# Kernel tuning notes

Hardware: AMD Instinct MI355X
Metric: run time of the kernel (lower is better)

The kernel has to match this reference:

```python
import jax, jax.numpy as jnp
import numpy as np

B, T, C = 4, 2048, 1024  # n_embd == input_size == 1024
H, D = 16, 64            # num_heads, head_size


def setup_inputs() -> dict:
    key = jax.random.key(0)
    ks = jax.random.split(key, 5)
    s_in = (1.0 / C) ** 0.5   # ~Linear default init scale
    s_pr = (1.0 / (H * D)) ** 0.5
    return {
        "x": jax.random.normal(ks[0], (B, T, C), dtype=jnp.float32),
        "wq": jax.random.normal(ks[1], (H, C, D), dtype=jnp.float32) * s_in,
        "wk": jax.random.normal(ks[2], (H, C, D), dtype=jnp.float32) * s_in,
        "wv": jax.random.normal(ks[3], (H, C, D), dtype=jnp.float32) * s_in,
        "w_proj": jax.random.normal(ks[4], (H * D, C), dtype=jnp.float32) * s_pr,
        "b_proj": jnp.zeros((C,), dtype=jnp.float32),
    }


def reference(x, wq, wk, wv, w_proj, b_proj):
    Bb, Tt, Cc = x.shape
    # Batched per-head projections: [B,T,C] x [H,C,D] -> [B,H,T,D]
    q = jnp.einsum("btc,hcd->bhtd", x, wq)
    k = jnp.einsum("btc,hcd->bhtd", x, wk)
    v = jnp.einsum("btc,hcd->bhtd", x, wv)
    # NOTE: original scales by C**-0.5 with C = full embedding dim (quirk preserved)
    scale = Cc ** (-0.5)
    scores = jnp.einsum("bhtd,bhsd->bhts", q, k) * scale  # [B,H,T,T]
    causal = jnp.tril(jnp.ones((Tt, Tt), dtype=bool))
    scores = jnp.where(causal, scores, -jnp.inf)
    wei = jax.nn.softmax(scores, axis=-1)
    out = jnp.einsum("bhts,bhsd->bhtd", wei, v)           # [B,H,T,D]
    out = out.transpose(0, 2, 1, 3).reshape(Bb, Tt, -1)    # concat heads [B,T,H*D]
    return out @ w_proj + b_proj                           # [B,T,C]
```

## Files before the change

kernel.cpp:

```cpp
#include <hip/hip_runtime.h>
#include <stdint.h>


typedef uint32_t u32;
typedef __bf16 bf16x8 __attribute__((ext_vector_type(8)));
typedef __bf16 bf16x4 __attribute__((ext_vector_type(4)));
typedef unsigned short us8 __attribute__((ext_vector_type(8)));
typedef float f32x4 __attribute__((ext_vector_type(4)));

#define EXP2F(x) __builtin_amdgcn_exp2f(x)

static __device__ __forceinline__ unsigned short f2bf(float f) {
  union { float f; u32 i; } cv; cv.f = f;
  u32 x = cv.i;
  u32 r = (x + 0x7fffu + ((x >> 16) & 1u)) >> 16;
  return (unsigned short)r;
}

static __device__ __forceinline__ void gload_lds16(const unsigned short* g, unsigned short* l) {
  __builtin_amdgcn_global_load_lds(
      (__attribute__((address_space(1))) u32*)g,
      (__attribute__((address_space(3))) u32*)l, 16, 0, 0);
}

#define G8_LGKM do { asm volatile("s_waitcnt lgkmcnt(0)" ::: "memory"); \
                     __builtin_amdgcn_sched_barrier(0); } while (0)

__global__ __launch_bounds__(256) void prep(
    const float* __restrict__ x, const float* __restrict__ wq,
    const float* __restrict__ wk, const float* __restrict__ wv,
    const float* __restrict__ wp, unsigned short* __restrict__ x_bf,
    unsigned short* __restrict__ wtq, unsigned short* __restrict__ wtp) {
  __shared__ unsigned short lds[64][66];
  const int b = blockIdx.x, tid = threadIdx.x;
  if (b < 4096) {
    size_t i = (size_t)(b * 256 + tid) * 8u;
    float4 a = *(const float4*)(x + i);
    float4 c = *(const float4*)(x + i + 4);
    us8 v;
    v[0] = f2bf(a.x); v[1] = f2bf(a.y); v[2] = f2bf(a.z); v[3] = f2bf(a.w);
    v[4] = f2bf(c.x); v[5] = f2bf(c.y); v[6] = f2bf(c.z); v[7] = f2bf(c.w);
    *(us8*)(x_bf + i) = v;
    return;
  }
  if (b < 4864) {
    int idx = b - 4096;
    int z = idx >> 8, rem = idx & 255;
    int h = rem >> 4, c0 = (rem & 15) << 6;
    const float* src = (z == 0) ? wq : (z == 1) ? wk : wv;
    unsigned short* d = wtq + ((size_t)z << 20);
    const float* s = src + (size_t)h * 65536u + (size_t)c0 * 64u;
#pragma unroll
    for (int it = 0; it < 16; ++it) {
      int i2 = it * 256 + tid;
      int r = i2 >> 6, dd = i2 & 63;
      lds[dd][r] = f2bf(s[r * 64 + dd]);
    }
    __syncthreads();
#pragma unroll
    for (int it = 0; it < 16; ++it) {
      int i2 = it * 256 + tid;
      int dd = i2 >> 6, r = i2 & 63;
      d[(size_t)(h * 64 + dd) * 1024u + c0 + r] = lds[dd][r];
    }
    return;
  }
  {
    int idx = b - 4864;
    int c0 = (idx >> 4) << 6, r0 = (idx & 15) << 6;
#pragma unroll
    for (int it = 0; it < 16; ++it) {
      int i2 = it * 256 + tid;
      int r = i2 >> 6, cc = i2 & 63;
      lds[cc][r] = f2bf(wp[(size_t)(r0 + r) * 1024u + c0 + cc]);
    }
    __syncthreads();
#pragma unroll
    for (int it = 0; it < 16; ++it) {
      int i2 = it * 256 + tid;
      int cc = i2 >> 6, r = i2 & 63;
      wtp[(size_t)(c0 + cc) * 1024u + r0 + r] = lds[cc][r];
    }
  }
}

static __device__ __forceinline__ void gn_stage(const unsigned short* g,
                                                unsigned short* d, int tid) {
#pragma unroll
  for (int l = 0; l < 4; ++l) {
    int cid = l * 256 + tid;
    int r = cid >> 3, c = cid & 7;
    gload_lds16(g + (size_t)r * 1024 + ((c ^ (r & 7)) << 3), d + cid * 8);
  }
}
static __device__ __forceinline__ void gn_ldA(bf16x8 af[4][2], const unsigned short* As,
                                              int wr, int l15, int lhi) {
#pragma unroll
  for (int mi = 0; mi < 4; ++mi)
#pragma unroll
    for (int ks = 0; ks < 2; ++ks) {
      int row = wr * 64 + mi * 16 + l15;
      af[mi][ks] = *(const bf16x8*)(As + row * 64 + ((((ks << 2) | lhi) ^ (row & 7)) << 3));
    }
}
static __device__ __forceinline__ void gn_ldB(bf16x8 bf[2][2], const unsigned short* Bs,
                                              int wc, int np, int l15, int lhi) {
#pragma unroll
  for (int ni = 0; ni < 2; ++ni)
#pragma unroll
    for (int ks = 0; ks < 2; ++ks) {
      int row = wc * 64 + np * 32 + ni * 16 + l15;
      bf[ni][ks] = *(const bf16x8*)(Bs + row * 64 + ((((ks << 2) | lhi) ^ (row & 7)) << 3));
    }
}
static __device__ __forceinline__ void gn_quad(f32x4 acc[4][4], bf16x8 af[4][2],
                                               bf16x8 bf[2][2], int np) {
#pragma unroll
  for (int ks = 0; ks < 2; ++ks)
#pragma unroll
    for (int mi = 0; mi < 4; ++mi)
#pragma unroll
      for (int ni = 0; ni < 2; ++ni)
        acc[mi][np * 2 + ni] = __builtin_amdgcn_mfma_f32_16x16x32_bf16(
            af[mi][ks], bf[ni][ks], acc[mi][np * 2 + ni], 0, 0, 0);
}

template <int F32OUT>
__global__ __launch_bounds__(256, 2) void gemmN(
    const unsigned short* __restrict__ A, const unsigned short* __restrict__ Bt,
    const float* __restrict__ bias, void* __restrict__ Cv,
    unsigned short* __restrict__ vt) {
  extern __shared__ __align__(16) unsigned short ldsm[];
  unsigned short* Ab = ldsm;
  unsigned short* Bb = ldsm + 16384;
  const int tid = threadIdx.x, wid = tid >> 6, lane = tid & 63;
  const int l15 = lane & 15, lhi = lane >> 4;
  const int wr = wid >> 1, wc = wid & 1;
  const int bid = blockIdx.x;
  const int mt = ((bid & 7) << 3) | ((bid >> 3) & 7);
  const int nt = bid >> 6;
  const int m0 = mt * 128, n0 = nt * 128;
  const unsigned short* Ag = A + (size_t)m0 * 1024;
  const unsigned short* Bg = Bt + (size_t)n0 * 1024;

  f32x4 acc[4][4] = {};
  bf16x8 af[4][2], b0[2][2], b1[2][2];

  gn_stage(Ag, Ab, tid);
  gn_stage(Bg, Bb, tid);
  asm volatile("s_waitcnt vmcnt(0)" ::: "memory");
  __builtin_amdgcn_s_barrier();

  for (int t = 0; t < 16; ++t) {
    const bool last = (t == 15);
    const int kc = t * 64;
    unsigned short* As = Ab + (t & 1) * 8192;
    unsigned short* Bs = Bb + (t & 1) * 8192;
    unsigned short* An = Ab + ((t & 1) ^ 1) * 8192;
    unsigned short* Bn = Bb + ((t & 1) ^ 1) * 8192;
    gn_ldA(af, As, wr, l15, lhi);
    gn_ldB(b0, Bs, wc, 0, l15, lhi);
    if (!last) gn_stage(Ag + (kc + 64), An, tid);
    __builtin_amdgcn_s_barrier(); G8_LGKM;
    __builtin_amdgcn_s_setprio(1); gn_quad(acc, af, b0, 0); __builtin_amdgcn_s_setprio(0);
    __builtin_amdgcn_s_barrier();
    gn_ldB(b1, Bs, wc, 1, l15, lhi);
    if (!last) gn_stage(Bg + (kc + 64), Bn, tid);
    __builtin_amdgcn_s_barrier(); G8_LGKM;
    __builtin_amdgcn_s_setprio(1); gn_quad(acc, af, b1, 1); __builtin_amdgcn_s_setprio(0);
    asm volatile("s_waitcnt vmcnt(0)" ::: "memory");
    __builtin_amdgcn_s_barrier();
  }

  if constexpr (!F32OUT) {
    if (nt >= 16) {
      unsigned short* tl = ldsm + wid * 4608;
#pragma unroll
      for (int mi = 0; mi < 4; ++mi)
#pragma unroll
        for (int ni = 0; ni < 4; ++ni)
#pragma unroll
          for (int r = 0; r < 4; ++r)
            tl[(ni * 16 + l15) * 72 + mi * 16 + lhi * 4 + r] = f2bf(acc[mi][ni][r]);
      asm volatile("s_waitcnt lgkmcnt(0)" ::: "memory");
      const int bb = m0 >> 11;
      const int bh = bb * 16 + (nt - 16) * 2 + wc;
      const int t0 = (m0 & 2047) + wr * 64;
      unsigned short* vrow = vt + (size_t)bh * 131072u + t0;
#pragma unroll
      for (int it = 0; it < 8; ++it) {
        int idx = it * 64 + lane;
        int dd = idx >> 3, tc = (idx & 7) << 3;
        *(us8*)(vrow + (size_t)dd * 2048u + tc) = *(const us8*)(tl + dd * 72 + tc);
      }
      return;
    }
  }

#pragma unroll
  for (int mi = 0; mi < 4; ++mi) {
#pragma unroll
    for (int ni = 0; ni < 4; ++ni) {
      const int n = n0 + wc * 64 + ni * 16 + l15;
      const int mr = m0 + wr * 64 + mi * 16 + lhi * 4;
      if constexpr (F32OUT) {
        float* O = (float*)Cv;
        const float b = bias[n];
#pragma unroll
        for (int r = 0; r < 4; ++r)
          O[(size_t)(mr + r) * 1024 + n] = acc[mi][ni][r] + b;
      } else {
        unsigned short* O = (unsigned short*)Cv + ((size_t)(n >> 10) << 23);
        const int nc = n & 1023;
#pragma unroll
        for (int r = 0; r < 4; ++r)
          O[(size_t)(mr + r) * 1024 + nc] = f2bf(acc[mi][ni][r]);
      }
    }
  }
}

#define QT 128
#define KVT 64
#define PSTR 72
#define SCLOG2E 0.04508422f

__global__ __launch_bounds__(512, 4) void attn_fwd(
    const unsigned short* __restrict__ Qg, const unsigned short* __restrict__ Kg,
    const unsigned short* __restrict__ Vtg, unsigned short* __restrict__ Og) {
  __shared__ __align__(16) unsigned short Kl[2][64 * 64];
  __shared__ __align__(16) unsigned short Vl[2][64 * 64];
  __shared__ __align__(16) unsigned short Pl[8][16 * PSTR];
  const int tid = threadIdx.x, wid = tid >> 6, lane = tid & 63;
  const int l15 = lane & 15, lhi = lane >> 4, x7 = lane & 7;
  const int bid = blockIdx.x;
  const int sub = bid & 63, pair = bid >> 6;
  const int bh = ((sub & 7) << 3) | (sub >> 3);
  const int qtA = pair, qtB = 15 - pair;
  const int n0 = 2 * (qtA + 1), n1 = 2 * (qtB + 1);
  const int ntot = n0 + n1;
  const size_t base = (size_t)(bh >> 4) * (2048u * 1024u) + (size_t)(bh & 15) * 64u;
  const size_t vtbase = (size_t)bh * 131072u;

  bf16x8 vones;
#pragma unroll
  for (int j = 0; j < 8; ++j) vones[j] = (__bf16)1.0f;

  auto s0_of = [&](int g) { return ((g < n0) ? g : g - n0) * KVT; };

  auto stage = [&](int bufi, int s0) {
    int q = tid;
    int r = q >> 3;
    int c = (q & 7) ^ (r & 7);
    gload_lds16(Kg + base + (size_t)(s0 + r) * 1024u + c * 8, &Kl[bufi][q * 8]);
    gload_lds16(Vtg + vtbase + (size_t)r * 2048u + s0 + c * 8, &Vl[bufi][q * 8]);
  };

  stage(0, 0);
  __syncthreads();

  int g = 0;
  for (int pass = 0; pass < 2; ++pass) {
    const int qt = pass ? qtB : qtA;
    const int nt = pass ? n1 : n0;
    const int qrow0 = qt * QT + wid * 16;

    bf16x8 qf[2];
#pragma unroll
    for (int kj = 0; kj < 2; ++kj)
      qf[kj] = *(const bf16x8*)(Qg + base +
          (size_t)(qrow0 + l15) * 1024u + kj * 32 + lhi * 8);

    f32x4 oacc[4] = {};
    f32x4 lacc = {};

    for (int kt = 0; kt < nt; ++kt, ++g) {
      const int cur = g & 1;
      const int s0 = kt * KVT;
      if (g + 1 < ntot) stage(cur ^ 1, s0_of(g + 1));
      if (s0 <= qrow0 + 15) {
        const bool notfull = (s0 + KVT - 1 > qrow0);
        const unsigned short* Kb = Kl[cur];
        const unsigned short* Vb = Vl[cur];

        f32x4 sacc[4] = {};
#pragma unroll
        for (int kj = 0; kj < 2; ++kj) {
          bf16x8 kf[4];
#pragma unroll
          for (int sj = 0; sj < 4; ++sj) {
            int r = sj * 16 + l15;
            kf[sj] = *(const bf16x8*)(&Kb[r * 64 + (((kj * 4 + lhi) ^ x7) * 8)]);
          }
#pragma unroll
          for (int sj = 0; sj < 4; ++sj)
            sacc[sj] = __builtin_amdgcn_mfma_f32_16x16x32_bf16(
                kf[sj], qf[kj], sacc[sj], 0, 0, 0);
        }

        if (notfull) {
          const int qa = qrow0 + l15;
#pragma unroll
          for (int sj = 0; sj < 4; ++sj)
#pragma unroll
            for (int r = 0; r < 4; ++r) {
              int sa = s0 + sj * 16 + lhi * 4 + r;
              sacc[sj][r] = (sa <= qa) ? sacc[sj][r] : -3e38f;
            }
        }

#pragma unroll
        for (int sj = 0; sj < 4; ++sj) {
          float p0 = EXP2F(sacc[sj][0] * SCLOG2E);
          float p1 = EXP2F(sacc[sj][1] * SCLOG2E);
          float p2 = EXP2F(sacc[sj][2] * SCLOG2E);
          float p3 = EXP2F(sacc[sj][3] * SCLOG2E);
          bf16x4 pk;
          pk[0] = (__bf16)p0; pk[1] = (__bf16)p1;
          pk[2] = (__bf16)p2; pk[3] = (__bf16)p3;
          *(bf16x4*)(&Pl[wid][l15 * PSTR + sj * 16 + lhi * 4]) = pk;
        }

#pragma unroll
        for (int kk = 0; kk < 2; ++kk) {
          bf16x8 pf, vf[4];
          pf = *(const bf16x8*)(&Pl[wid][l15 * PSTR + kk * 32 + lhi * 8]);
#pragma unroll
          for (int dj = 0; dj < 4; ++dj) {
            int r = dj * 16 + l15;
            vf[dj] = *(const bf16x8*)(&Vb[r * 64 + (((kk * 4 + lhi) ^ x7) * 8)]);
          }
#pragma unroll
          for (int dj = 0; dj < 4; ++dj)
            oacc[dj] = __builtin_amdgcn_mfma_f32_16x16x32_bf16(
                pf, vf[dj], oacc[dj], 0, 0, 0);
          lacc = __builtin_amdgcn_mfma_f32_16x16x32_bf16(pf, vones, lacc, 0, 0, 0);
        }
      }

      __syncthreads();
    }

    float rn[4];
#pragma unroll
    for (int r = 0; r < 4; ++r) rn[r] = 1.0f / lacc[r];
#pragma unroll
    for (int dj = 0; dj < 4; ++dj)
#pragma unroll
      for (int r = 0; r < 4; ++r) {
        int t = qrow0 + lhi * 4 + r;
        Og[base + (size_t)t * 1024u + dj * 16 + l15] = f2bf(oacc[dj][r] * rn[r]);
      }
  }
}

extern "C" void kernel_launch(void* const* d_in, const int* in_sizes, int n_in,
                              void* d_out, int out_size, void* d_ws, size_t ws_size,
                              hipStream_t stream) {
  const float* x  = (const float*)d_in[0];
  const float* wq = (const float*)d_in[1];
  const float* wk = (const float*)d_in[2];
  const float* wv = (const float*)d_in[3];
  const float* wp = (const float*)d_in[4];
  const float* bp = (const float*)d_in[5];
  float* out = (float*)d_out;

  unsigned short* ws   = (unsigned short*)d_ws;
  unsigned short* x_bf = ws;
  unsigned short* wtq  = ws + ((size_t)8 << 20);
  unsigned short* wtp  = ws + ((size_t)11 << 20);
  unsigned short* qkv  = ws + ((size_t)12 << 20);
  unsigned short* q    = qkv;
  unsigned short* kk   = qkv + ((size_t)8 << 20);
  unsigned short* att  = qkv + ((size_t)16 << 20);
  unsigned short* vt   = ws + ((size_t)36 << 20);

  (void)hipFuncSetAttribute(reinterpret_cast<const void*>(&gemmN<0>),
                            hipFuncAttributeMaxDynamicSharedMemorySize, 65536);
  (void)hipFuncSetAttribute(reinterpret_cast<const void*>(&gemmN<1>),
                            hipFuncAttributeMaxDynamicSharedMemorySize, 65536);

  prep<<<5120, 256, 0, stream>>>(x, wq, wk, wv, wp, x_bf, wtq, wtp);
  gemmN<0><<<1536, 256, 65536, stream>>>(x_bf, wtq, nullptr, qkv, vt);
  attn_fwd<<<512, 512, 0, stream>>>(q, kk, vt, att);
  gemmN<1><<<512, 256, 65536, stream>>>(att, wtp, bp, out, nullptr);
}
```

Baseline: 143.2 us.

## Load GEMM B operand directly from global into registers, bypass LDS

The GEMM kernel no longer stages the B (weight) tile through LDS. Each wave loads its B fragments straight from global memory into registers, double-buffered across even and odd K-steps, while A is still staged through LDS. Per-iteration barriers drop from four to two and the LDS allocation shrinks, which may raise occupancy. In exchange, B fragment loads are strided global reads (1024-element row stride, 16 bytes per lane) that each wave repeats without sharing through LDS, and register pressure rises from holding two full B fragment sets.

```diff
diff --git a/kernel.cpp b/kernel.cpp
--- a/kernel.cpp
+++ b/kernel.cpp
@@ -103,26 +103,25 @@
       af[mi][ks] = *(const bf16x8*)(As + row * 64 + ((((ks << 2) | lhi) ^ (row & 7)) << 3));
     }
 }
-static __device__ __forceinline__ void gn_ldB(bf16x8 bf[2][2], const unsigned short* Bs,
-                                              int wc, int np, int l15, int lhi) {
-#pragma unroll
-  for (int ni = 0; ni < 2; ++ni)
-#pragma unroll
-    for (int ks = 0; ks < 2; ++ks) {
-      int row = wc * 64 + np * 32 + ni * 16 + l15;
-      bf[ni][ks] = *(const bf16x8*)(Bs + row * 64 + ((((ks << 2) | lhi) ^ (row & 7)) << 3));
-    }
-}
-static __device__ __forceinline__ void gn_quad(f32x4 acc[4][4], bf16x8 af[4][2],
-                                               bf16x8 bf[2][2], int np) {
+static __device__ __forceinline__ void gn_ldBg(bf16x8 br[4][2], const unsigned short* Bg,
+                                               int wc, int kc, int l15, int lhi) {
+#pragma unroll
+  for (int ni = 0; ni < 4; ++ni)
+#pragma unroll
+    for (int ks = 0; ks < 2; ++ks)
+      br[ni][ks] = *(const bf16x8*)(Bg +
+          (size_t)(wc * 64 + ni * 16 + l15) * 1024 + kc + ks * 32 + lhi * 8);
+}
+static __device__ __forceinline__ void gn_all(f32x4 acc[4][4], bf16x8 af[4][2],
+                                              bf16x8 br[4][2]) {
 #pragma unroll
   for (int ks = 0; ks < 2; ++ks)
 #pragma unroll
     for (int mi = 0; mi < 4; ++mi)
 #pragma unroll
-      for (int ni = 0; ni < 2; ++ni)
-        acc[mi][np * 2 + ni] = __builtin_amdgcn_mfma_f32_16x16x32_bf16(
-            af[mi][ks], bf[ni][ks], acc[mi][np * 2 + ni], 0, 0, 0);
+      for (int ni = 0; ni < 4; ++ni)
+        acc[mi][ni] = __builtin_amdgcn_mfma_f32_16x16x32_bf16(
+            af[mi][ks], br[ni][ks], acc[mi][ni], 0, 0, 0);
 }
 
 template <int F32OUT>
@@ -132,7 +131,6 @@
     unsigned short* __restrict__ vt) {
   extern __shared__ __align__(16) unsigned short ldsm[];
   unsigned short* Ab = ldsm;
-  unsigned short* Bb = ldsm + 16384;
   const int tid = threadIdx.x, wid = tid >> 6, lane = tid & 63;
   const int l15 = lane & 15, lhi = lane >> 4;
   const int wr = wid >> 1, wc = wid & 1;
@@ -144,31 +142,31 @@
   const unsigned short* Bg = Bt + (size_t)n0 * 1024;
 
   f32x4 acc[4][4] = {};
-  bf16x8 af[4][2], b0[2][2], b1[2][2];
-
+  bf16x8 af[4][2], bEven[4][2], bOdd[4][2];
+
+  gn_ldBg(bEven, Bg, wc, 0, l15, lhi);
   gn_stage(Ag, Ab, tid);
-  gn_stage(Bg, Bb, tid);
   asm volatile("s_waitcnt vmcnt(0)" ::: "memory");
   __builtin_amdgcn_s_barrier();
 
-  for (int t = 0; t < 16; ++t) {
-    const bool last = (t == 15);
-    const int kc = t * 64;
-    unsigned short* As = Ab + (t & 1) * 8192;
-    unsigned short* Bs = Bb + (t & 1) * 8192;
-    unsigned short* An = Ab + ((t & 1) ^ 1) * 8192;
-    unsigned short* Bn = Bb + ((t & 1) ^ 1) * 8192;
-    gn_ldA(af, As, wr, l15, lhi);
-    gn_ldB(b0, Bs, wc, 0, l15, lhi);
-    if (!last) gn_stage(Ag + (kc + 64), An, tid);
-    __builtin_amdgcn_s_barrier(); G8_LGKM;
-    __builtin_amdgcn_s_setprio(1); gn_quad(acc, af, b0, 0); __builtin_amdgcn_s_setprio(0);
+  for (int j = 0; j < 8; ++j) {
+    const int kc = j * 128;
+    const bool lastj = (j == 7);
+    gn_ldA(af, Ab, wr, l15, lhi);
+    gn_ldBg(bOdd, Bg, wc, kc + 64, l15, lhi);
+    gn_stage(Ag + (kc + 64), Ab + 8192, tid);
+    G8_LGKM;
+    __builtin_amdgcn_s_setprio(1); gn_all(acc, af, bEven); __builtin_amdgcn_s_setprio(0);
+    asm volatile("s_waitcnt vmcnt(0)" ::: "memory");
     __builtin_amdgcn_s_barrier();
-    gn_ldB(b1, Bs, wc, 1, l15, lhi);
-    if (!last) gn_stage(Bg + (kc + 64), Bn, tid);
-    __builtin_amdgcn_s_barrier(); G8_LGKM;
-    __builtin_amdgcn_s_setprio(1); gn_quad(acc, af, b1, 1); __builtin_amdgcn_s_setprio(0);
-    asm volatile("s_waitcnt vmcnt(0)" ::: "memory");
+    gn_ldA(af, Ab + 8192, wr, l15, lhi);
+    if (!lastj) {
+      gn_ldBg(bEven, Bg, wc, kc + 128, l15, lhi);
+      gn_stage(Ag + (kc + 128), Ab, tid);
+    }
+    G8_LGKM;
+    __builtin_amdgcn_s_setprio(1); gn_all(acc, af, bOdd); __builtin_amdgcn_s_setprio(0);
+    if (!lastj) asm volatile("s_waitcnt vmcnt(0)" ::: "memory");
     __builtin_amdgcn_s_barrier();
   }
 
@@ -376,12 +374,12 @@
   unsigned short* vt   = ws + ((size_t)36 << 20);
 
   (void)hipFuncSetAttribute(reinterpret_cast<const void*>(&gemmN<0>),
-                            hipFuncAttributeMaxDynamicSharedMemorySize, 65536);
+                            hipFuncAttributeMaxDynamicSharedMemorySize, 40960);
   (void)hipFuncSetAttribute(reinterpret_cast<const void*>(&gemmN<1>),
-                            hipFuncAttributeMaxDynamicSharedMemorySize, 65536);
+                            hipFuncAttributeMaxDynamicSharedMemorySize, 40960);
 
   prep<<<5120, 256, 0, stream>>>(x, wq, wk, wv, wp, x_bf, wtq, wtp);
-  gemmN<0><<<1536, 256, 65536, stream>>>(x_bf, wtq, nullptr, qkv, vt);
+  gemmN<0><<<1536, 256, 40960, stream>>>(x_bf, wtq, nullptr, qkv, vt);
   attn_fwd<<<512, 512, 0, stream>>>(q, kk, vt, att);
-  gemmN<1><<<512, 256, 65536, stream>>>(att, wtp, bp, out, nullptr);
-}
+  gemmN<1><<<512, 256, 40960, stream>>>(att, wtp, bp, out, nullptr);
+}
```

Result: slower. 212.2 us (+48.2%).

## Process both paired query tiles in one KV sweep, sharing K/V tiles

Applied to the files above, without the earlier changes.

The causal attention kernel used to run two sequential passes per block, one per paired query tile, and stage the KV prefix twice. It now loads both query tiles up front and makes a single sweep over the longer tile's KV range. Each staged K/V tile and its register fragments are reused for both query sets, with the short tile dropping out once it is past its causal limit. This roughly removes one set of KV global loads and barriers per block, at the cost of more live registers (two sets of Q fragments and accumulators plus all K/V fragments) under launch bounds (512, 4).

```diff
diff --git a/kernel.cpp b/kernel.cpp
--- a/kernel.cpp
+++ b/kernel.cpp
@@ -237,16 +237,15 @@
   const int sub = bid & 63, pair = bid >> 6;
   const int bh = ((sub & 7) << 3) | (sub >> 3);
   const int qtA = pair, qtB = 15 - pair;
-  const int n0 = 2 * (qtA + 1), n1 = 2 * (qtB + 1);
-  const int ntot = n0 + n1;
+  const int ntB = 2 * (qtB + 1);
   const size_t base = (size_t)(bh >> 4) * (2048u * 1024u) + (size_t)(bh & 15) * 64u;
   const size_t vtbase = (size_t)bh * 131072u;
+  const int qrow0A = qtA * QT + wid * 16;
+  const int qrow0B = qtB * QT + wid * 16;
 
   bf16x8 vones;
 #pragma unroll
   for (int j = 0; j < 8; ++j) vones[j] = (__bf16)1.0f;
-
-  auto s0_of = [&](int g) { return ((g < n0) ? g : g - n0) * KVT; };
 
   auto stage = [&](int bufi, int s0) {
     int q = tid;
@@ -256,91 +255,107 @@
     gload_lds16(Vtg + vtbase + (size_t)r * 2048u + s0 + c * 8, &Vl[bufi][q * 8]);
   };
 
+  bf16x8 qfA[2], qfB[2];
+#pragma unroll
+  for (int kj = 0; kj < 2; ++kj) {
+    qfA[kj] = *(const bf16x8*)(Qg + base +
+        (size_t)(qrow0A + l15) * 1024u + kj * 32 + lhi * 8);
+    qfB[kj] = *(const bf16x8*)(Qg + base +
+        (size_t)(qrow0B + l15) * 1024u + kj * 32 + lhi * 8);
+  }
+
+  f32x4 oaccA[4] = {}, oaccB[4] = {};
+  f32x4 laccA = {}, laccB = {};
+
   stage(0, 0);
   __syncthreads();
 
-  int g = 0;
-  for (int pass = 0; pass < 2; ++pass) {
-    const int qt = pass ? qtB : qtA;
-    const int nt = pass ? n1 : n0;
-    const int qrow0 = qt * QT + wid * 16;
-
-    bf16x8 qf[2];
+  for (int kt = 0; kt < ntB; ++kt) {
+    const int cur = kt & 1;
+    const int s0 = kt * KVT;
+    if (kt + 1 < ntB) stage(cur ^ 1, (kt + 1) * KVT);
+    const unsigned short* Kb = Kl[cur];
+    const unsigned short* Vb = Vl[cur];
+
+    const bool actA = (s0 <= qrow0A + 15);
+    const bool actB = (s0 <= qrow0B + 15);
+
+    bf16x8 kf[2][4];
 #pragma unroll
     for (int kj = 0; kj < 2; ++kj)
-      qf[kj] = *(const bf16x8*)(Qg + base +
-          (size_t)(qrow0 + l15) * 1024u + kj * 32 + lhi * 8);
-
-    f32x4 oacc[4] = {};
-    f32x4 lacc = {};
-
-    for (int kt = 0; kt < nt; ++kt, ++g) {
-      const int cur = g & 1;
-      const int s0 = kt * KVT;
-      if (g + 1 < ntot) stage(cur ^ 1, s0_of(g + 1));
-      if (s0 <= qrow0 + 15) {
-        const bool notfull = (s0 + KVT - 1 > qrow0);
-        const unsigned short* Kb = Kl[cur];
-        const unsigned short* Vb = Vl[cur];
-
-        f32x4 sacc[4] = {};
-#pragma unroll
-        for (int kj = 0; kj < 2; ++kj) {
-          bf16x8 kf[4];
-#pragma unroll
-          for (int sj = 0; sj < 4; ++sj) {
-            int r = sj * 16 + l15;
-            kf[sj] = *(const bf16x8*)(&Kb[r * 64 + (((kj * 4 + lhi) ^ x7) * 8)]);
+#pragma unroll
+      for (int sj = 0; sj < 4; ++sj) {
+        int r = sj * 16 + l15;
+        kf[kj][sj] = *(const bf16x8*)(&Kb[r * 64 + (((kj * 4 + lhi) ^ x7) * 8)]);
+      }
+    bf16x8 vf[2][4];
+#pragma unroll
+    for (int kk = 0; kk < 2; ++kk)
+#pragma unroll
+      for (int dj = 0; dj < 4; ++dj) {
+        int r = dj * 16 + l15;
+        vf[kk][dj] = *(const bf16x8*)(&Vb[r * 64 + (((kk * 4 + lhi) ^ x7) * 8)]);
+      }
+
+#pragma unroll
+    for (int set = 0; set < 2; ++set) {
+      const bool act = set ? actB : actA;
+      if (!act) continue;
+      const int qrow0 = set ? qrow0B : qrow0A;
+      const bf16x8* qf = set ? qfB : qfA;
+      f32x4* oacc = set ? oaccB : oaccA;
+      f32x4& lacc = set ? laccB : laccA;
+
+      f32x4 sacc[4] = {};
+#pragma unroll
+      for (int kj = 0; kj < 2; ++kj)
+#pragma unroll
+        for (int sj = 0; sj < 4; ++sj)
+          sacc[sj] = __builtin_amdgcn_mfma_f32_16x16x32_bf16(
+              kf[kj][sj], qf[kj], sacc[sj], 0, 0, 0);
+
+      if (s0 + KVT - 1 > qrow0) {
+        const int qa = qrow0 + l15;
+#pragma unroll
+        for (int sj = 0; sj < 4; ++sj)
+#pragma unroll
+          for (int r = 0; r < 4; ++r) {
+            int sa = s0 + sj * 16 + lhi * 4 + r;
+            sacc[sj][r] = (sa <= qa) ? sacc[sj][r] : -3e38f;
           }
-#pragma unroll
-          for (int sj = 0; sj < 4; ++sj)
-            sacc[sj] = __builtin_amdgcn_mfma_f32_16x16x32_bf16(
-                kf[sj], qf[kj], sacc[sj], 0, 0, 0);
-        }
-
-        if (notfull) {
-          const int qa = qrow0 + l15;
-#pragma unroll
-          for (int sj = 0; sj < 4; ++sj)
-#pragma unroll
-            for (int r = 0; r < 4; ++r) {
-              int sa = s0 + sj * 16 + lhi * 4 + r;
-              sacc[sj][r] = (sa <= qa) ? sacc[sj][r] : -3e38f;
-            }
-        }
-
-#pragma unroll
-        for (int sj = 0; sj < 4; ++sj) {
-          float p0 = EXP2F(sacc[sj][0] * SCLOG2E);
-          float p1 = EXP2F(sacc[sj][1] * SCLOG2E);
-          float p2 = EXP2F(sacc[sj][2] * SCLOG2E);
-          float p3 = EXP2F(sacc[sj][3] * SCLOG2E);
-          bf16x4 pk;
-          pk[0] = (__bf16)p0; pk[1] = (__bf16)p1;
-          pk[2] = (__bf16)p2; pk[3] = (__bf16)p3;
-          *(bf16x4*)(&Pl[wid][l15 * PSTR + sj * 16 + lhi * 4]) = pk;
-        }
-
-#pragma unroll
-        for (int kk = 0; kk < 2; ++kk) {
-          bf16x8 pf, vf[4];
-          pf = *(const bf16x8*)(&Pl[wid][l15 * PSTR + kk * 32 + lhi * 8]);
-#pragma unroll
-          for (int dj = 0; dj < 4; ++dj) {
-            int r = dj * 16 + l15;
-            vf[dj] = *(const bf16x8*)(&Vb[r * 64 + (((kk * 4 + lhi) ^ x7) * 8)]);
-          }
-#pragma unroll
-          for (int dj = 0; dj < 4; ++dj)
-            oacc[dj] = __builtin_amdgcn_mfma_f32_16x16x32_bf16(
-                pf, vf[dj], oacc[dj], 0, 0, 0);
-          lacc = __builtin_amdgcn_mfma_f32_16x16x32_bf16(pf, vones, lacc, 0, 0, 0);
-        }
-      }
-
-      __syncthreads();
-    }
-
+      }
+
+#pragma unroll
+      for (int sj = 0; sj < 4; ++sj) {
+        float p0 = EXP2F(sacc[sj][0] * SCLOG2E);
+        float p1 = EXP2F(sacc[sj][1] * SCLOG2E);
+        float p2 = EXP2F(sacc[sj][2] * SCLOG2E);
+        float p3 = EXP2F(sacc[sj][3] * SCLOG2E);
+        bf16x4 pk;
+        pk[0] = (__bf16)p0; pk[1] = (__bf16)p1;
+        pk[2] = (__bf16)p2; pk[3] = (__bf16)p3;
+        *(bf16x4*)(&Pl[wid][l15 * PSTR + sj * 16 + lhi * 4]) = pk;
+      }
+
+#pragma unroll
+      for (int kk = 0; kk < 2; ++kk) {
+        bf16x8 pf = *(const bf16x8*)(&Pl[wid][l15 * PSTR + kk * 32 + lhi * 8]);
+#pragma unroll
+        for (int dj = 0; dj < 4; ++dj)
+          oacc[dj] = __builtin_amdgcn_mfma_f32_16x16x32_bf16(
+              pf, vf[kk][dj], oacc[dj], 0, 0, 0);
+        lacc = __builtin_amdgcn_mfma_f32_16x16x32_bf16(pf, vones, lacc, 0, 0, 0);
+      }
+    }
+
+    __syncthreads();
+  }
+
+#pragma unroll
+  for (int set = 0; set < 2; ++set) {
+    const int qrow0 = set ? qrow0B : qrow0A;
+    f32x4* oacc = set ? oaccB : oaccA;
+    f32x4& lacc = set ? laccB : laccA;
     float rn[4];
 #pragma unroll
     for (int r = 0; r < 4; ++r) rn[r] = 1.0f / lacc[r];
```

Measured after the change: 295.7 us. 107% more time.

## Process two KV tiles per barrier with four-slot staging and swizzled P buffer

Applied to the files above, without the earlier changes.

The attention loop now stages two KV tiles at a time into a four-slot LDS ring and computes two tiles between each barrier, halving the number of __syncthreads calls and prefetching further ahead. The P scratch buffer drops its padded stride in favour of an XOR swizzle to avoid LDS bank conflicts. LDS use roughly doubles for K/V, which may cut occupancy under the 512x4 launch bounds.

```diff
diff --git a/kernel.cpp b/kernel.cpp
--- a/kernel.cpp
+++ b/kernel.cpp
@@ -222,15 +222,14 @@
 
 #define QT 128
 #define KVT 64
-#define PSTR 72
 #define SCLOG2E 0.04508422f
 
 __global__ __launch_bounds__(512, 4) void attn_fwd(
     const unsigned short* __restrict__ Qg, const unsigned short* __restrict__ Kg,
     const unsigned short* __restrict__ Vtg, unsigned short* __restrict__ Og) {
-  __shared__ __align__(16) unsigned short Kl[2][64 * 64];
-  __shared__ __align__(16) unsigned short Vl[2][64 * 64];
-  __shared__ __align__(16) unsigned short Pl[8][16 * PSTR];
+  __shared__ __align__(16) unsigned short Kl[4][64 * 64];
+  __shared__ __align__(16) unsigned short Vl[4][64 * 64];
+  __shared__ __align__(16) unsigned short Pl[8][16 * 64];
   const int tid = threadIdx.x, wid = tid >> 6, lane = tid & 63;
   const int l15 = lane & 15, lhi = lane >> 4, x7 = lane & 7;
   const int bid = blockIdx.x;
@@ -248,15 +247,16 @@
 
   auto s0_of = [&](int g) { return ((g < n0) ? g : g - n0) * KVT; };
 
-  auto stage = [&](int bufi, int s0) {
+  auto stage = [&](int slot, int s0) {
     int q = tid;
     int r = q >> 3;
     int c = (q & 7) ^ (r & 7);
-    gload_lds16(Kg + base + (size_t)(s0 + r) * 1024u + c * 8, &Kl[bufi][q * 8]);
-    gload_lds16(Vtg + vtbase + (size_t)r * 2048u + s0 + c * 8, &Vl[bufi][q * 8]);
+    gload_lds16(Kg + base + (size_t)(s0 + r) * 1024u + c * 8, &Kl[slot][q * 8]);
+    gload_lds16(Vtg + vtbase + (size_t)r * 2048u + s0 + c * 8, &Vl[slot][q * 8]);
   };
 
-  stage(0, 0);
+  stage(0, s0_of(0));
+  stage(1, s0_of(1));
   __syncthreads();
 
   int g = 0;
@@ -274,70 +274,75 @@
     f32x4 oacc[4] = {};
     f32x4 lacc = {};
 
-    for (int kt = 0; kt < nt; ++kt, ++g) {
-      const int cur = g & 1;
-      const int s0 = kt * KVT;
-      if (g + 1 < ntot) stage(cur ^ 1, s0_of(g + 1));
-      if (s0 <= qrow0 + 15) {
-        const bool notfull = (s0 + KVT - 1 > qrow0);
-        const unsigned short* Kb = Kl[cur];
-        const unsigned short* Vb = Vl[cur];
-
-        f32x4 sacc[4] = {};
-#pragma unroll
-        for (int kj = 0; kj < 2; ++kj) {
-          bf16x8 kf[4];
-#pragma unroll
-          for (int sj = 0; sj < 4; ++sj) {
-            int r = sj * 16 + l15;
-            kf[sj] = *(const bf16x8*)(&Kb[r * 64 + (((kj * 4 + lhi) ^ x7) * 8)]);
+    auto do_tile = [&](int s0, const unsigned short* Kb, const unsigned short* Vb) {
+      if (s0 > qrow0 + 15) return;
+      const bool notfull = (s0 + KVT - 1 > qrow0);
+
+      f32x4 sacc[4] = {};
+#pragma unroll
+      for (int kj = 0; kj < 2; ++kj) {
+        bf16x8 kf[4];
+#pragma unroll
+        for (int sj = 0; sj < 4; ++sj) {
+          int r = sj * 16 + l15;
+          kf[sj] = *(const bf16x8*)(&Kb[r * 64 + (((kj * 4 + lhi) ^ x7) * 8)]);
+        }
+#pragma unroll
+        for (int sj = 0; sj < 4; ++sj)
+          sacc[sj] = __builtin_amdgcn_mfma_f32_16x16x32_bf16(
+              kf[sj], qf[kj], sacc[sj], 0, 0, 0);
+      }
+
+      if (notfull) {
+        const int qa = qrow0 + l15;
+#pragma unroll
+        for (int sj = 0; sj < 4; ++sj)
+#pragma unroll
+          for (int r = 0; r < 4; ++r) {
+            int sa = s0 + sj * 16 + lhi * 4 + r;
+            sacc[sj][r] = (sa <= qa) ? sacc[sj][r] : -3e38f;
           }
-#pragma unroll
-          for (int sj = 0; sj < 4; ++sj)
-            sacc[sj] = __builtin_amdgcn_mfma_f32_16x16x32_bf16(
-                kf[sj], qf[kj], sacc[sj], 0, 0, 0);
+      }
+
+#pragma unroll
+      for (int sj = 0; sj < 4; ++sj) {
+        float p0 = EXP2F(sacc[sj][0] * SCLOG2E);
+        float p1 = EXP2F(sacc[sj][1] * SCLOG2E);
+        float p2 = EXP2F(sacc[sj][2] * SCLOG2E);
+        float p3 = EXP2F(sacc[sj][3] * SCLOG2E);
+        bf16x4 pk;
+        pk[0] = (__bf16)p0; pk[1] = (__bf16)p1;
+        pk[2] = (__bf16)p2; pk[3] = (__bf16)p3;
+        int wch = ((2 * sj + (lhi >> 1)) ^ (l15 & 7)) << 3;
+        *(bf16x4*)(&Pl[wid][l15 * 64 + wch + (lhi & 1) * 4]) = pk;
+      }
+
+#pragma unroll
+      for (int kk = 0; kk < 2; ++kk) {
+        bf16x8 pf, vf[4];
+        pf = *(const bf16x8*)(&Pl[wid][l15 * 64 + ((((kk << 2) | lhi) ^ (l15 & 7)) << 3)]);
+#pragma unroll
+        for (int dj = 0; dj < 4; ++dj) {
+          int r = dj * 16 + l15;
+          vf[dj] = *(const bf16x8*)(&Vb[r * 64 + (((kk * 4 + lhi) ^ x7) * 8)]);
         }
-
-        if (notfull) {
-          const int qa = qrow0 + l15;
-#pragma unroll
-          for (int sj = 0; sj < 4; ++sj)
-#pragma unroll
-            for (int r = 0; r < 4; ++r) {
-              int sa = s0 + sj * 16 + lhi * 4 + r;
-              sacc[sj][r] = (sa <= qa) ? sacc[sj][r] : -3e38f;
-            }
-        }
-
-#pragma unroll
-        for (int sj = 0; sj < 4; ++sj) {
-          float p0 = EXP2F(sacc[sj][0] * SCLOG2E);
-          float p1 = EXP2F(sacc[sj][1] * SCLOG2E);
-          float p2 = EXP2F(sacc[sj][2] * SCLOG2E);
-          float p3 = EXP2F(sacc[sj][3] * SCLOG2E);
-          bf16x4 pk;
-          pk[0] = (__bf16)p0; pk[1] = (__bf16)p1;
-          pk[2] = (__bf16)p2; pk[3] = (__bf16)p3;
-          *(bf16x4*)(&Pl[wid][l15 * PSTR + sj * 16 + lhi * 4]) = pk;
-        }
-
-#pragma unroll
-        for (int kk = 0; kk < 2; ++kk) {
-          bf16x8 pf, vf[4];
-          pf = *(const bf16x8*)(&Pl[wid][l15 * PSTR + kk * 32 + lhi * 8]);
-#pragma unroll
-          for (int dj = 0; dj < 4; ++dj) {
-            int r = dj * 16 + l15;
-            vf[dj] = *(const bf16x8*)(&Vb[r * 64 + (((kk * 4 + lhi) ^ x7) * 8)]);
-          }
-#pragma unroll
-          for (int dj = 0; dj < 4; ++dj)
-            oacc[dj] = __builtin_amdgcn_mfma_f32_16x16x32_bf16(
-                pf, vf[dj], oacc[dj], 0, 0, 0);
-          lacc = __builtin_amdgcn_mfma_f32_16x16x32_bf16(pf, vones, lacc, 0, 0, 0);
-        }
-      }
-
+#pragma unroll
+        for (int dj = 0; dj < 4; ++dj)
+          oacc[dj] = __builtin_amdgcn_mfma_f32_16x16x32_bf16(
+              pf, vf[dj], oacc[dj], 0, 0, 0);
+        lacc = __builtin_amdgcn_mfma_f32_16x16x32_bf16(pf, vones, lacc, 0, 0, 0);
+      }
+    };
+
+    for (int kt = 0; kt < nt; kt += 2, g += 2) {
+      const int sb = ((g >> 1) & 1) << 1;
+      const int nb = sb ^ 2;
+      if (g + 2 < ntot) {
+        stage(nb, s0_of(g + 2));
+        if (g + 3 < ntot) stage(nb + 1, s0_of(g + 3));
+      }
+      do_tile(kt * KVT, Kl[sb], Vl[sb]);
+      do_tile((kt + 1) * KVT, Kl[sb + 1], Vl[sb + 1]);
       __syncthreads();
     }
 
```

Result: no change. 143.0 us, median of 2 (-0.1%).
